# Optimization experiments

Measured on AMD Instinct MI355X. Metric: run time of the kernel, lower is better.

The kernel has to match this reference:

```python
import jax, jax.numpy as jnp
import numpy as np

DEVICE_DIM, SERVER_DIM, HIDDEN, HEAD_HIDDEN = 14, 3, 64, 128
B, N_DEV = 16384, 63
N_NODES = N_DEV + 1


def setup_inputs() -> dict:
    key = jax.random.key(0)
    ks = jax.random.split(key, 16)
    device_obs = jax.random.normal(ks[0], (B, N_DEV, DEVICE_DIM), dtype=jnp.float32)
    server_obs = jax.random.normal(ks[1], (B, SERVER_DIM), dtype=jnp.float32)
    # binary adjacency with self-loops (as built by _dense_adjacency_from_edge_index)
    rand = jax.random.uniform(ks[2], (B, N_NODES, N_NODES))
    adjacency = jnp.clip((rand < 0.3).astype(jnp.float32) + jnp.eye(N_NODES, dtype=jnp.float32), 0.0, 1.0)

    def lin(k, fan_in, fan_out):
        w = jax.random.normal(k, (fan_in, fan_out), dtype=jnp.float32) / np.sqrt(fan_in)
        return w

    return {
        'device_obs': device_obs,
        'server_obs': server_obs,
        'adjacency': adjacency,
        'W_dev': lin(ks[3], DEVICE_DIM, HIDDEN), 'b_dev': jnp.zeros((HIDDEN,), jnp.float32),
        'W_srv': lin(ks[4], SERVER_DIM, HIDDEN), 'b_srv': jnp.zeros((HIDDEN,), jnp.float32),
        'W1': lin(ks[5], HIDDEN, HIDDEN), 'b1': jnp.zeros((HIDDEN,), jnp.float32),
        'W2': lin(ks[6], HIDDEN, HIDDEN), 'b2': jnp.zeros((HIDDEN,), jnp.float32),
        'W3': lin(ks[7], HIDDEN, HIDDEN), 'b3': jnp.zeros((HIDDEN,), jnp.float32),
        'Wf1': lin(ks[8], HIDDEN * 3, HEAD_HIDDEN), 'bf1': jnp.zeros((HEAD_HIDDEN,), jnp.float32),
        'Wf2': lin(ks[9], HEAD_HIDDEN, 1), 'bf2': jnp.zeros((1,), jnp.float32),
    }


def _dense_gcn(x, adj_norm, W, b):
    # normalized adjacency matmul then linear: [B,N,N]@[B,N,H] -> [B,N,H]
    return jnp.einsum('bnm,bmh->bnh', adj_norm, x) @ W + b


def reference(device_obs, server_obs, adjacency,
              W_dev, b_dev, W_srv, b_srv,
              W1, b1, W2, b2, W3, b3,
              Wf1, bf1, Wf2, bf2):
    # node encoding
    device_emb = jax.nn.relu(device_obs @ W_dev + b_dev)            # [B,Nd,H]
    server_emb = jax.nn.relu(server_obs @ W_srv + b_srv)[:, None]   # [B,1,H]
    x = jnp.concatenate([device_emb, server_emb], axis=1)           # [B,N,H]

    # symmetric degree normalization D^-1/2 A D^-1/2 (degree clamped to >=1)
    degree = adjacency.sum(axis=-1)
    d_inv_sqrt = jnp.clip(degree, 1.0, None) ** -0.5
    adj_norm = d_inv_sqrt[:, :, None] * adjacency * d_inv_sqrt[:, None, :]

    h = jax.nn.relu(_dense_gcn(x, adj_norm, W1, b1))
    h = jax.nn.relu(_dense_gcn(h, adj_norm, W2, b2))
    h = jax.nn.relu(_dense_gcn(h, adj_norm, W3, b3))

    # head
    server_hidden = h[:, -1]                  # [B,H]
    device_hidden = h[:, :-1]                 # [B,Nd,H]
    dev_mean = device_hidden.mean(axis=1)     # [B,H]
    n = device_hidden.shape[1]
    shared_srv = jnp.broadcast_to(server_hidden[:, None], (h.shape[0], n, HIDDEN))
    shared_mean = jnp.broadcast_to(dev_mean[:, None], (h.shape[0], n, HIDDEN))
    critic_in = jnp.concatenate([device_hidden, shared_mean, shared_srv], axis=-1)  # [B,Nd,3H]
    out = jax.nn.relu(critic_in @ Wf1 + bf1) @ Wf2 + bf2
    return out[..., 0]  # [B,Nd]
```

## Files before the change

### kernel.cpp

```cpp
#include <hip/hip_runtime.h>
#include <hip/hip_bf16.h>
#include <stdint.h>

typedef __attribute__((ext_vector_type(8))) __bf16 bf16x8;
typedef __attribute__((ext_vector_type(4))) float f32x4;
typedef __attribute__((ext_vector_type(2))) float f32x2;
typedef __attribute__((ext_vector_type(4))) unsigned uint4v;
typedef __attribute__((ext_vector_type(2))) unsigned uint2v;

union U4 { uint4v u; bf16x8 b; };

#define WS_WDEV_H 0
#define WS_WDEV_L 4096
#define WS_W1_H   8192
#define WS_W1_L   16384
#define WS_W2_H   24576
#define WS_W2_L   32768
#define WS_W3_H   40960
#define WS_W3_L   49152
#define WS_WA_H   57344
#define WS_WA_L   73728
#define WS_WF_H   90112
#define WS_WF_L   122880

__device__ __forceinline__ unsigned short f2bf(float f){
  union { float f; unsigned u; } v; v.f = f;
  unsigned r = v.u + 0x7fffu + ((v.u >> 16) & 1u);
  return (unsigned short)(r >> 16);
}
__device__ __forceinline__ float bf2f(unsigned short h){
  union { unsigned u; float f; } v; v.u = ((unsigned)h) << 16; return v.f;
}
__device__ __forceinline__ void split2(float x, unsigned short& hi, unsigned short& lo){
  hi = f2bf(x);
  lo = f2bf(x - bf2f(hi));
}
__device__ __forceinline__ f32x4 mfma16(const U4& a, const U4& b, f32x4 c){
  return __builtin_amdgcn_mfma_f32_16x16x32_bf16(a.b, b.b, c, 0, 0, 0);
}

__device__ __forceinline__ unsigned cvt_pk_bf(float a, float b){
  float2 p; p.x = a; p.y = b;
  union { __hip_bfloat162 h; unsigned u; } cv;
  cv.h = __float22bfloat162_rn(p);
  return cv.u;
}
__device__ __forceinline__ void split_pair(float x0, float x1, unsigned& hi2, unsigned& lo2){
  hi2 = cvt_pk_bf(x0, x1);
  lo2 = cvt_pk_bf(x0 - __uint_as_float(hi2 << 16),
                  x1 - __uint_as_float(hi2 & 0xffff0000u));
}
__device__ __forceinline__ unsigned pack_hl(float z){
  unsigned h = cvt_pk_bf(z, 0.f) & 0xffffu;
  float r = z - __uint_as_float(h << 16);
  return (cvt_pk_bf(0.f, r) & 0xffff0000u) | h;
}

extern "C" __global__ void prep_weights(const float* __restrict__ Wdev,
                                        const float* __restrict__ W1,
                                        const float* __restrict__ W2,
                                        const float* __restrict__ W3,
                                        const float* __restrict__ Wf1,
                                        char* __restrict__ ws)
{
  unsigned short* WdevH = (unsigned short*)(ws + WS_WDEV_H);
  unsigned short* WdevL = (unsigned short*)(ws + WS_WDEV_L);
  unsigned short* WH[3] = {(unsigned short*)(ws+WS_W1_H),(unsigned short*)(ws+WS_W2_H),(unsigned short*)(ws+WS_W3_H)};
  unsigned short* WL[3] = {(unsigned short*)(ws+WS_W1_L),(unsigned short*)(ws+WS_W2_L),(unsigned short*)(ws+WS_W3_L)};
  unsigned short* WaH = (unsigned short*)(ws + WS_WA_H);
  unsigned short* WaL = (unsigned short*)(ws + WS_WA_L);
  unsigned short* WfH = (unsigned short*)(ws + WS_WF_H);
  unsigned short* WfL = (unsigned short*)(ws + WS_WF_L);
  const int total = 2048 + 3*4096 + 8192 + 16384;
  for (int idx = blockIdx.x*256 + threadIdx.x; idx < total; idx += gridDim.x*256){
    if (idx < 2048){
      int tt = idx;
      int frag = tt >> 9, within = tt & 511, lane = within >> 3, j = within & 7;
      int nt = frag & 3;
      int k = ((lane>>4)<<3) + j;
      int n = (nt<<4) + (lane & 15);
      float v = (k < 14) ? Wdev[k*64 + n] : 0.f;
      unsigned short h,l; split2(v,h,l); WdevH[tt]=h; WdevL[tt]=l;
    } else if (idx < 2048 + 3*4096){
      int tt = idx - 2048; int Li = tt / 4096; int r = tt - Li*4096;
      int frag = r >> 9, within = r & 511, lane = within >> 3, j = within & 7;
      int ks = frag >> 2, nt = frag & 3;
      int k = (ks<<5) + ((lane>>4)<<3) + j;
      int n = (nt<<4) + (lane & 15);
      const float* W = (Li==0) ? W1 : ((Li==1) ? W2 : W3);
      float v = W[k*64 + n];
      unsigned short h,l; split2(v,h,l); WH[Li][r]=h; WL[Li][r]=l;
    } else if (idx < 2048 + 3*4096 + 8192){
      int r = idx - (2048 + 3*4096);
      int frag = r >> 9, within = r & 511, lane = within >> 3, j = within & 7;
      int ks = frag >> 3, nt = frag & 7;
      int k = (ks<<5) + ((lane>>4)<<3) + j;
      int n = (nt<<4) + (lane & 15);
      float v = Wf1[k*128 + n];
      unsigned short h,l; split2(v,h,l); WaH[r]=h; WaL[r]=l;
    } else {
      int r = idx - (2048 + 3*4096 + 8192);
      int frag = r >> 9, within = r & 511, lane = within >> 3, j = within & 7;
      int ks = frag >> 3, nt = frag & 7;
      int k = (ks<<5) + ((lane>>4)<<3) + j;
      int n = (nt<<4) + (lane & 15);
      float v = Wf1[(64 + k)*128 + n];
      unsigned short h,l; split2(v,h,l); WfH[r]=h; WfL[r]=l;
    }
  }
}

extern "C" __global__ __launch_bounds__(256, 6)
void pgcn_fused(const float* __restrict__ dobs, const float* __restrict__ sobs,
                const float* __restrict__ adj,
                const float* __restrict__ bdev,
                const float* __restrict__ Wsrv, const float* __restrict__ bsrv,
                const float* __restrict__ b1, const float* __restrict__ b2,
                const float* __restrict__ b3,
                const float* __restrict__ bf1, const float* __restrict__ Wf2,
                const float* __restrict__ bf2,
                const char* __restrict__ ws, float* __restrict__ out)
{
  __shared__ __align__(16) unsigned short     lds_Yr[9216];
  __shared__ __align__(16) unsigned long long lds_Abits[64];
  __shared__ __align__(16) float    lds_d[64];
  __shared__ __align__(16) float    lds_mp[256];
  __shared__ __align__(16) float    lds_srv[64];
  __shared__ __align__(16) float    lds_s1[128];
  __shared__ __align__(16) unsigned short lds_Vh[128];
  __shared__ __align__(16) unsigned short lds_Vl[128];

  const int t = threadIdx.x;
  const int w = t >> 6;
  const int lane = t & 63;
  const int quad = lane >> 4;
  const int c = lane & 15;
  const long item = blockIdx.x;
  char* Yb = (char*)lds_Yr;

  {
    const f32x4* src = (const f32x4*)(adj + item*4096 + ((t>>2)<<6) + ((t&3)<<4));
    unsigned bits = 0;
    for (int i = 0; i < 4; ++i){
      f32x4 v = src[i];
      unsigned b = (v.x != 0.f) | (((unsigned)(v.y != 0.f))<<1)
                 | (((unsigned)(v.z != 0.f))<<2) | (((unsigned)(v.w != 0.f))<<3);
      bits |= b << (i<<2);
    }
    ((unsigned short*)lds_Abits)[t] = (unsigned short)bits;
  }

  unsigned ahi[4] = {0,0,0,0}, alo[4] = {0,0,0,0};
  {
    int m = (w<<4) + c;
    if (quad < 2 && m < 63){
      const float* rp = dobs + item*882 + m*14 + (quad<<3);
      float e[8];
      f32x2 p0 = *(const f32x2*)(rp);
      f32x2 p1 = *(const f32x2*)(rp+2);
      f32x2 p2 = *(const f32x2*)(rp+4);
      e[0]=p0.x; e[1]=p0.y; e[2]=p1.x; e[3]=p1.y; e[4]=p2.x; e[5]=p2.y;
      if (quad == 0){
        f32x2 p3 = *(const f32x2*)(rp+6);
        e[6]=p3.x; e[7]=p3.y;
      } else {
        e[6]=0.f; e[7]=0.f;
      }
      for (int d0 = 0; d0 < 4; ++d0)
        split_pair(e[2*d0], e[2*d0+1], ahi[d0], alo[d0]);
    }
  }
  __syncthreads();

  if (t < 64){
    unsigned long long mk = lds_Abits[t];
    int deg = __popcll(mk);
    lds_d[t] = 1.0f / sqrtf((float)(deg < 1 ? 1 : deg));
  }
  __syncthreads();

  f32x4 d4v = *(const f32x4*)&lds_d[(w<<4) + (quad<<2)];
  const float dd[4] = {d4v.x, d4v.y, d4v.z, d4v.w};
  const float ddc = lds_d[(w<<4) + c];

  U4 atk[2];
  {
    unsigned long long mk = lds_Abits[(w<<4) + c];
    for (int ks = 0; ks < 2; ++ks){
      unsigned byt = (unsigned)(mk >> ((ks<<5) + (quad<<3))) & 0xffu;
      for (int r = 0; r < 4; ++r){
        unsigned e = 0u - ((byt >> (2*r)) & 1u);
        unsigned o = 0u - ((byt >> (2*r+1)) & 1u);
        atk[ks].u[r] = (e & 0x3f80u) | (o & 0x3f800000u);
      }
    }
  }

  const int ybw = (c*72 + (w<<4) + (quad<<2)) << 1;
  const int yrd = (c*72 + (quad<<3)) << 1;
  const int zbw = (((w<<4)+c)*72 + (quad<<2)) << 1;
  const int zrd = (((w<<4)+c)*72 + (quad<<3)) << 1;

  float hcur[4][4];

  {
    U4 a_h, a_l;
    a_h.u = uint4v{ahi[0],ahi[1],ahi[2],ahi[3]};
    a_l.u = uint4v{alo[0],alo[1],alo[2],alo[3]};
    const uint4v* WdH = (const uint4v*)(ws + WS_WDEV_H);
    const uint4v* WdL = (const uint4v*)(ws + WS_WDEV_L);
    float srvv4[4];
    if (w == 3 && quad == 3){
      float s0 = sobs[item*3+0], s1v = sobs[item*3+1], s2v = sobs[item*3+2];
      for (int nt = 0; nt < 4; ++nt){
        int col = c + (nt<<4);
        float v = s0*Wsrv[col] + s1v*Wsrv[64+col] + s2v*Wsrv[128+col] + bsrv[col];
        srvv4[nt] = fmaxf(v, 0.f);
      }
    }
    for (int nt = 0; nt < 4; ++nt){
      U4 wh, wl;
      wh.u = WdH[(nt<<6) + lane];
      wl.u = WdL[(nt<<6) + lane];
      f32x4 g = {0.f,0.f,0.f,0.f};
      g = mfma16(a_h, wh, g);
      g = mfma16(a_h, wl, g);
      g = mfma16(a_l, wh, g);
      float bb = bdev[c + (nt<<4)];
      float y[4];
      for (int r = 0; r < 4; ++r) y[r] = fmaxf(g[r] + bb, 0.f);
      if (w == 3 && quad == 3) y[3] = srvv4[nt];
      for (int r = 0; r < 4; ++r) y[r] *= dd[r];
      unsigned h01, l01, h23, l23;
      split_pair(y[0], y[1], h01, l01);
      split_pair(y[2], y[3], h23, l23);
      *(uint2v*)(Yb + ybw + 2304*nt)        = uint2v{ h01, h23 };
      *(uint2v*)(Yb + ybw + 2304*nt + 9216) = uint2v{ l01, l23 };
    }
  }
  __syncthreads();

  const uint4v* WH_tab[3] = {(const uint4v*)(ws+WS_W1_H),(const uint4v*)(ws+WS_W2_H),(const uint4v*)(ws+WS_W3_H)};
  const uint4v* WL_tab[3] = {(const uint4v*)(ws+WS_W1_L),(const uint4v*)(ws+WS_W2_L),(const uint4v*)(ws+WS_W3_L)};
  const float* bias_tab[3] = {b1, b2, b3};

  for (int L = 0; L < 3; ++L){
    f32x4 zacc[4];
    for (int mt = 0; mt < 4; ++mt){
      f32x4 g = {0.f,0.f,0.f,0.f};
      for (int ks = 0; ks < 2; ++ks){
        U4 yh, yl;
        yh.u = *(const uint4v*)(Yb + yrd + 2304*mt + 64*ks);
        yl.u = *(const uint4v*)(Yb + yrd + 2304*mt + 64*ks + 9216);
        g = mfma16(yh, atk[ks], g);
        g = mfma16(yl, atk[ks], g);
      }
      zacc[mt] = g;
    }
    __syncthreads();

    for (int mt = 0; mt < 4; ++mt){
      unsigned h01, l01, h23, l23;
      split_pair(zacc[mt][0]*ddc, zacc[mt][1]*ddc, h01, l01);
      split_pair(zacc[mt][2]*ddc, zacc[mt][3]*ddc, h23, l23);
      *(uint2v*)(Yb + zbw + 32*mt)        = uint2v{ h01, h23 };
      *(uint2v*)(Yb + zbw + 32*mt + 9216) = uint2v{ l01, l23 };
    }
    __threadfence_block();
    U4 zh[2], zl[2];
    for (int ks = 0; ks < 2; ++ks){
      zh[ks].u = *(const uint4v*)(Yb + zrd + 64*ks);
      zl[ks].u = *(const uint4v*)(Yb + zrd + 64*ks + 9216);
    }

    const uint4v* WHp = WH_tab[L];
    const uint4v* WLp = WL_tab[L];
    const float* bp = bias_tab[L];
    for (int nt = 0; nt < 4; ++nt){
      f32x4 g = {0.f,0.f,0.f,0.f};
      for (int ks = 0; ks < 2; ++ks){
        U4 wh, wl;
        wh.u = WHp[((ks<<2)+nt)*64 + lane];
        wl.u = WLp[((ks<<2)+nt)*64 + lane];
        g = mfma16(zh[ks], wh, g);
        g = mfma16(zh[ks], wl, g);
        g = mfma16(zl[ks], wh, g);
      }
      float bb = bp[c + (nt<<4)];
      for (int r = 0; r < 4; ++r) hcur[nt][r] = fmaxf(g[r] + bb, 0.f);
    }
    __syncthreads();

    if (L < 2){
      for (int nt = 0; nt < 4; ++nt){
        unsigned h01, l01, h23, l23;
        split_pair(hcur[nt][0]*dd[0], hcur[nt][1]*dd[1], h01, l01);
        split_pair(hcur[nt][2]*dd[2], hcur[nt][3]*dd[3], h23, l23);
        *(uint2v*)(Yb + ybw + 2304*nt)        = uint2v{ h01, h23 };
        *(uint2v*)(Yb + ybw + 2304*nt + 9216) = uint2v{ l01, l23 };
      }
      __syncthreads();
    }
  }

  unsigned* zbuf = (unsigned*)Yb + (w<<10);
  const int piL = (lane>>2) | ((lane&3)<<4);
  const int s0L = (piL>>2) & 1;

  {
    bool isSrvLane = (w == 3) && (quad == 3);
    float cs[4];
    for (int nt = 0; nt < 4; ++nt){
      float s = hcur[nt][0] + hcur[nt][1] + hcur[nt][2] + hcur[nt][3];
      if (isSrvLane){ s -= hcur[nt][3]; lds_srv[c + (nt<<4)] = hcur[nt][3]; }
      s += __shfl_xor(s, 16);
      s += __shfl_xor(s, 32);
      cs[nt] = s;
    }
    if (quad == 0)
      for (int nt = 0; nt < 4; ++nt) lds_mp[(w<<6) + c + (nt<<4)] = cs[nt];
  }
  for (int nt = 0; nt < 4; ++nt){
    int ks = nt >> 1;
    int lcBase = (quad<<2) + ((((nt&1)<<1) + (c>>3)) << 4);
    int e = c & 7;
    for (int r = 0; r < 4; ++r){
      unsigned pk = pack_hl(hcur[nt][r]);
      int lane_c = lcBase + r;
      int pi = (lane_c>>2) | ((lane_c&3)<<4);
      int sel = ((e>>2) ^ (pi>>2)) & 1;
      zbuf[(ks<<9) + (pi<<3) + (sel<<2) + (e&3)] = pk;
    }
  }
  __syncthreads();

  if (t < 64){
    float mv = (lds_mp[t] + lds_mp[64+t] + lds_mp[128+t] + lds_mp[192+t]) * (1.0f/63.0f);
    unsigned short h,l; split2(mv,h,l);
    lds_Vh[t]=h; lds_Vl[t]=l;
  } else if (t < 128){
    float sv = lds_srv[t-64];
    unsigned short h,l; split2(sv,h,l);
    lds_Vh[t]=h; lds_Vl[t]=l;
  }
  __syncthreads();

  U4 hh[2], hl[2];
  for (int ks = 0; ks < 2; ++ks){
    uint4v qa = *(const uint4v*)&zbuf[(ks<<9) + (piL<<3) + (s0L<<2)];
    uint4v qb = *(const uint4v*)&zbuf[(ks<<9) + (piL<<3) + ((1-s0L)<<2)];
    hh[ks].u = uint4v{ (qa.y<<16)|(qa.x&0xffffu), (qa.w<<16)|(qa.z&0xffffu),
                       (qb.y<<16)|(qb.x&0xffffu), (qb.w<<16)|(qb.z&0xffffu) };
    hl[ks].u = uint4v{ (qa.y&0xffff0000u)|(qa.x>>16), (qa.w&0xffff0000u)|(qa.z>>16),
                       (qb.y&0xffff0000u)|(qb.x>>16), (qb.w&0xffff0000u)|(qb.z>>16) };
  }

  {
    const uint4v* WfH = (const uint4v*)(ws + WS_WF_H);
    const uint4v* WfL = (const uint4v*)(ws + WS_WF_L);
    f32x4 sacc0 = {0.f,0.f,0.f,0.f}, sacc1 = {0.f,0.f,0.f,0.f};
    for (int ks = 0; ks < 4; ++ks){
      U4 vh, vl;
      vh.u = *(const uint4v*)((const char*)lds_Vh + (ks<<6) + (quad<<4));
      vl.u = *(const uint4v*)((const char*)lds_Vl + (ks<<6) + (quad<<4));
      if (c != 0){ vh.u = uint4v{0,0,0,0}; vl.u = uint4v{0,0,0,0}; }
      int nt0 = (w<<1);
      U4 wh, wl;
      wh.u = WfH[((ks<<3)+nt0)*64 + lane];
      wl.u = WfL[((ks<<3)+nt0)*64 + lane];
      sacc0 = mfma16(vh, wh, sacc0);
      sacc0 = mfma16(vh, wl, sacc0);
      sacc0 = mfma16(vl, wh, sacc0);
      wh.u = WfH[((ks<<3)+nt0+1)*64 + lane];
      wl.u = WfL[((ks<<3)+nt0+1)*64 + lane];
      sacc1 = mfma16(vh, wh, sacc1);
      sacc1 = mfma16(vh, wl, sacc1);
      sacc1 = mfma16(vl, wh, sacc1);
    }
    if (quad == 0){
      int col0 = c + (w<<5);
      lds_s1[col0]      = sacc0[0] + bf1[col0];
      lds_s1[col0 + 16] = sacc1[0] + bf1[col0 + 16];
    }
  }
  __syncthreads();

  const uint4v* WaH = (const uint4v*)(ws + WS_WA_H);
  const uint4v* WaL = (const uint4v*)(ws + WS_WA_L);
  float outacc[4] = {0.f,0.f,0.f,0.f};
  for (int nt = 0; nt < 8; ++nt){
    f32x4 g = {0.f,0.f,0.f,0.f};
    for (int ks = 0; ks < 2; ++ks){
      U4 wh, wl;
      wh.u = WaH[((ks<<3)+nt)*64 + lane];
      wl.u = WaL[((ks<<3)+nt)*64 + lane];
      g = mfma16(hh[ks], wh, g);
      g = mfma16(hh[ks], wl, g);
      g = mfma16(hl[ks], wh, g);
    }
    int col = c + (nt<<4);
    float sv = lds_s1[col];
    float w2 = Wf2[col];
    for (int r = 0; r < 4; ++r){
      float zz = fmaxf(g[r] + sv, 0.f);
      outacc[r] += zz * w2;
    }
  }
  {
    float bb = bf2[0];
    for (int r = 0; r < 4; ++r){
      float v = outacc[r];
      v += __shfl_xor(v, 1); v += __shfl_xor(v, 2);
      v += __shfl_xor(v, 4); v += __shfl_xor(v, 8);
      if (c == 0){
        int row = (w<<4) + (quad<<2) + r;
        if (row < 63) out[item*63 + row] = v + bb;
      }
    }
  }
}

extern "C" void kernel_launch(void* const* d_in, const int* in_sizes, int n_in,
                              void* d_out, int out_size, void* d_ws, size_t ws_size,
                              hipStream_t stream)
{
  const float* dobs = (const float*)d_in[0];
  const float* sobs = (const float*)d_in[1];
  const float* adj  = (const float*)d_in[2];
  const float* Wdev = (const float*)d_in[3];
  const float* bdev = (const float*)d_in[4];
  const float* Wsrv = (const float*)d_in[5];
  const float* bsrv = (const float*)d_in[6];
  const float* W1   = (const float*)d_in[7];
  const float* b1   = (const float*)d_in[8];
  const float* W2   = (const float*)d_in[9];
  const float* b2   = (const float*)d_in[10];
  const float* W3   = (const float*)d_in[11];
  const float* b3   = (const float*)d_in[12];
  const float* Wf1  = (const float*)d_in[13];
  const float* bf1  = (const float*)d_in[14];
  const float* Wf2  = (const float*)d_in[15];
  const float* bf2  = (const float*)d_in[16];
  float* out = (float*)d_out;
  char* ws = (char*)d_ws;
  int nb = in_sizes[1] / 3;

  prep_weights<<<dim3(160), dim3(256), 0, stream>>>(Wdev, W1, W2, W3, Wf1, ws);
  pgcn_fused<<<dim3(nb), dim3(256), 0, stream>>>(dobs, sobs, adj, bdev, Wsrv, bsrv,
                                                 b1, b2, b3, bf1, Wf2, bf2, ws, out);
}
```

Baseline: 628.9 us.

## Software-pipeline weight and LDS loads with double buffering across GCN and head stages

Manually unrolls the embedding, GCN layer, and head MFMA loops so the weight fragments from the workspace and the LDS operands for the next tile load while the current tile's MFMAs run. Bias, Wf2, and server-encoding loads are hoisted earlier so their latency overlaps other work. The adjacency is read with nontemporal loads, and the block fence is replaced by an explicit lgkmcnt wait. The launch-bounds occupancy hint drops from 6 to 5 to leave room for the extra live registers, which may reduce latency hiding across waves.

```diff
diff --git a/kernel.cpp b/kernel.cpp
--- a/kernel.cpp
+++ b/kernel.cpp
@@ -110,7 +110,7 @@
   }
 }
 
-extern "C" __global__ __launch_bounds__(256, 6)
+extern "C" __global__ __launch_bounds__(256, 5)
 void pgcn_fused(const float* __restrict__ dobs, const float* __restrict__ sobs,
                 const float* __restrict__ adj,
                 const float* __restrict__ bdev,
@@ -137,12 +137,13 @@
   const int c = lane & 15;
   const long item = blockIdx.x;
   char* Yb = (char*)lds_Yr;
+  const bool isSrv = (w == 3) && (quad == 3);
 
   {
     const f32x4* src = (const f32x4*)(adj + item*4096 + ((t>>2)<<6) + ((t&3)<<4));
     unsigned bits = 0;
     for (int i = 0; i < 4; ++i){
-      f32x4 v = src[i];
+      f32x4 v = __builtin_nontemporal_load(src + i);
       unsigned b = (v.x != 0.f) | (((unsigned)(v.y != 0.f))<<1)
                  | (((unsigned)(v.z != 0.f))<<2) | (((unsigned)(v.w != 0.f))<<3);
       bits |= b << (i<<2);
@@ -170,6 +171,18 @@
         split_pair(e[2*d0], e[2*d0+1], ahi[d0], alo[d0]);
     }
   }
+
+  float bdv0 = bdev[c], bdv1 = bdev[c+16], bdv2 = bdev[c+32], bdv3 = bdev[c+48];
+  float srvv4[4];
+  if (isSrv){
+    float s0 = sobs[item*3+0], s1a = sobs[item*3+1], s2a = sobs[item*3+2];
+#pragma unroll
+    for (int nt = 0; nt < 4; ++nt){
+      int col = c + (nt<<4);
+      float v = s0*Wsrv[col] + s1a*Wsrv[64+col] + s2a*Wsrv[128+col] + bsrv[col];
+      srvv4[nt] = fmaxf(v, 0.f);
+    }
+  }
   __syncthreads();
 
   if (t < 64){
@@ -207,36 +220,34 @@
     U4 a_h, a_l;
     a_h.u = uint4v{ahi[0],ahi[1],ahi[2],ahi[3]};
     a_l.u = uint4v{alo[0],alo[1],alo[2],alo[3]};
-    const uint4v* WdH = (const uint4v*)(ws + WS_WDEV_H);
-    const uint4v* WdL = (const uint4v*)(ws + WS_WDEV_L);
-    float srvv4[4];
-    if (w == 3 && quad == 3){
-      float s0 = sobs[item*3+0], s1v = sobs[item*3+1], s2v = sobs[item*3+2];
-      for (int nt = 0; nt < 4; ++nt){
-        int col = c + (nt<<4);
-        float v = s0*Wsrv[col] + s1v*Wsrv[64+col] + s2v*Wsrv[128+col] + bsrv[col];
-        srvv4[nt] = fmaxf(v, 0.f);
-      }
-    }
-    for (int nt = 0; nt < 4; ++nt){
-      U4 wh, wl;
-      wh.u = WdH[(nt<<6) + lane];
-      wl.u = WdL[(nt<<6) + lane];
-      f32x4 g = {0.f,0.f,0.f,0.f};
-      g = mfma16(a_h, wh, g);
-      g = mfma16(a_h, wl, g);
-      g = mfma16(a_l, wh, g);
-      float bb = bdev[c + (nt<<4)];
-      float y[4];
-      for (int r = 0; r < 4; ++r) y[r] = fmaxf(g[r] + bb, 0.f);
-      if (w == 3 && quad == 3) y[3] = srvv4[nt];
-      for (int r = 0; r < 4; ++r) y[r] *= dd[r];
-      unsigned h01, l01, h23, l23;
-      split_pair(y[0], y[1], h01, l01);
-      split_pair(y[2], y[3], h23, l23);
-      *(uint2v*)(Yb + ybw + 2304*nt)        = uint2v{ h01, h23 };
-      *(uint2v*)(Yb + ybw + 2304*nt + 9216) = uint2v{ l01, l23 };
-    }
+    const uint4v* WdHp = (const uint4v*)(ws + WS_WDEV_H);
+    const uint4v* WdLp = (const uint4v*)(ws + WS_WDEV_L);
+    U4 eAh, eAl, eBh, eBl;
+    eAh.u = WdHp[0*64 + lane]; eAl.u = WdLp[0*64 + lane];
+    eBh.u = WdHp[1*64 + lane]; eBl.u = WdLp[1*64 + lane];
+#define EMB(NT, WHF, WLF, BB) { \
+    f32x4 g = {0.f,0.f,0.f,0.f}; \
+    g = mfma16(a_h, WHF, g); \
+    g = mfma16(a_h, WLF, g); \
+    g = mfma16(a_l, WHF, g); \
+    float y0 = fmaxf(g[0] + (BB), 0.f); \
+    float y1 = fmaxf(g[1] + (BB), 0.f); \
+    float y2 = fmaxf(g[2] + (BB), 0.f); \
+    float y3 = fmaxf(g[3] + (BB), 0.f); \
+    if (isSrv) y3 = srvv4[NT];             \
+    y0 *= dd[0]; y1 *= dd[1]; y2 *= dd[2]; y3 *= dd[3];    \
+    unsigned h01,l01,h23,l23; \
+    split_pair(y0, y1, h01, l01); \
+    split_pair(y2, y3, h23, l23); \
+    *(uint2v*)(Yb + ybw + 2304*(NT))        = uint2v{ h01, h23 }; \
+    *(uint2v*)(Yb + ybw + 2304*(NT) + 9216) = uint2v{ l01, l23 }; }
+    EMB(0, eAh, eAl, bdv0)
+    eAh.u = WdHp[2*64 + lane]; eAl.u = WdLp[2*64 + lane];
+    EMB(1, eBh, eBl, bdv1)
+    eBh.u = WdHp[3*64 + lane]; eBl.u = WdLp[3*64 + lane];
+    EMB(2, eAh, eAl, bdv2)
+    EMB(3, eBh, eBl, bdv3)
+#undef EMB
   }
   __syncthreads();
 
@@ -245,50 +256,90 @@
   const float* bias_tab[3] = {b1, b2, b3};
 
   for (int L = 0; L < 3; ++L){
-    f32x4 zacc[4];
-    for (int mt = 0; mt < 4; ++mt){
-      f32x4 g = {0.f,0.f,0.f,0.f};
-      for (int ks = 0; ks < 2; ++ks){
-        U4 yh, yl;
-        yh.u = *(const uint4v*)(Yb + yrd + 2304*mt + 64*ks);
-        yl.u = *(const uint4v*)(Yb + yrd + 2304*mt + 64*ks + 9216);
-        g = mfma16(yh, atk[ks], g);
-        g = mfma16(yl, atk[ks], g);
-      }
-      zacc[mt] = g;
-    }
-    __syncthreads();
-
-    for (int mt = 0; mt < 4; ++mt){
-      unsigned h01, l01, h23, l23;
-      split_pair(zacc[mt][0]*ddc, zacc[mt][1]*ddc, h01, l01);
-      split_pair(zacc[mt][2]*ddc, zacc[mt][3]*ddc, h23, l23);
-      *(uint2v*)(Yb + zbw + 32*mt)        = uint2v{ h01, h23 };
-      *(uint2v*)(Yb + zbw + 32*mt + 9216) = uint2v{ l01, l23 };
-    }
-    __threadfence_block();
-    U4 zh[2], zl[2];
-    for (int ks = 0; ks < 2; ++ks){
-      zh[ks].u = *(const uint4v*)(Yb + zrd + 64*ks);
-      zl[ks].u = *(const uint4v*)(Yb + zrd + 64*ks + 9216);
-    }
-
     const uint4v* WHp = WH_tab[L];
     const uint4v* WLp = WL_tab[L];
     const float* bp = bias_tab[L];
-    for (int nt = 0; nt < 4; ++nt){
-      f32x4 g = {0.f,0.f,0.f,0.f};
-      for (int ks = 0; ks < 2; ++ks){
-        U4 wh, wl;
-        wh.u = WHp[((ks<<2)+nt)*64 + lane];
-        wl.u = WLp[((ks<<2)+nt)*64 + lane];
-        g = mfma16(zh[ks], wh, g);
-        g = mfma16(zh[ks], wl, g);
-        g = mfma16(zl[ks], wh, g);
-      }
-      float bb = bp[c + (nt<<4)];
-      for (int r = 0; r < 4; ++r) hcur[nt][r] = fmaxf(g[r] + bb, 0.f);
-    }
+    float bL0 = bp[c], bL1 = bp[c+16], bL2 = bp[c+32], bL3 = bp[c+48];
+
+    f32x4 zacc0, zacc1, zacc2, zacc3;
+    {
+      U4 yAh0,yAl0,yAh1,yAl1, yBh0,yBl0,yBh1,yBl1;
+#define LOADY(H0,L0,H1,L1, MT) \
+      H0.u = *(const uint4v*)(Yb + yrd + 2304*(MT)); \
+      L0.u = *(const uint4v*)(Yb + yrd + 2304*(MT) + 9216); \
+      H1.u = *(const uint4v*)(Yb + yrd + 2304*(MT) + 64); \
+      L1.u = *(const uint4v*)(Yb + yrd + 2304*(MT) + 64 + 9216);
+#define ZSTEP(ZD, H0,L0,H1,L1) { \
+      f32x4 g = {0.f,0.f,0.f,0.f}; \
+      g = mfma16(H0, atk[0], g); \
+      g = mfma16(L0, atk[0], g); \
+      g = mfma16(H1, atk[1], g); \
+      g = mfma16(L1, atk[1], g); \
+      ZD = g; }
+      LOADY(yAh0,yAl0,yAh1,yAl1, 0)
+      LOADY(yBh0,yBl0,yBh1,yBl1, 1)
+      ZSTEP(zacc0, yAh0,yAl0,yAh1,yAl1)
+      LOADY(yAh0,yAl0,yAh1,yAl1, 2)
+      ZSTEP(zacc1, yBh0,yBl0,yBh1,yBl1)
+      LOADY(yBh0,yBl0,yBh1,yBl1, 3)
+      ZSTEP(zacc2, yAh0,yAl0,yAh1,yAl1)
+      ZSTEP(zacc3, yBh0,yBl0,yBh1,yBl1)
+#undef LOADY
+#undef ZSTEP
+    }
+    __syncthreads();
+
+    U4 wAh0,wAl0,wAh1,wAl1, wBh0,wBl0,wBh1,wBl1;
+#define LOADW(H0,L0,H1,L1, NT) \
+    H0.u = WHp[(NT)*64 + lane]; \
+    L0.u = WLp[(NT)*64 + lane]; \
+    H1.u = WHp[(4+(NT))*64 + lane]; \
+    L1.u = WLp[(4+(NT))*64 + lane];
+    LOADW(wAh0,wAl0,wAh1,wAl1, 0)
+
+    {
+      unsigned h01,l01,h23,l23;
+      split_pair(zacc0[0]*ddc, zacc0[1]*ddc, h01, l01);
+      split_pair(zacc0[2]*ddc, zacc0[3]*ddc, h23, l23);
+      *(uint2v*)(Yb + zbw +  0)        = uint2v{ h01, h23 };
+      *(uint2v*)(Yb + zbw +  0 + 9216) = uint2v{ l01, l23 };
+      split_pair(zacc1[0]*ddc, zacc1[1]*ddc, h01, l01);
+      split_pair(zacc1[2]*ddc, zacc1[3]*ddc, h23, l23);
+      *(uint2v*)(Yb + zbw + 32)        = uint2v{ h01, h23 };
+      *(uint2v*)(Yb + zbw + 32 + 9216) = uint2v{ l01, l23 };
+      split_pair(zacc2[0]*ddc, zacc2[1]*ddc, h01, l01);
+      split_pair(zacc2[2]*ddc, zacc2[3]*ddc, h23, l23);
+      *(uint2v*)(Yb + zbw + 64)        = uint2v{ h01, h23 };
+      *(uint2v*)(Yb + zbw + 64 + 9216) = uint2v{ l01, l23 };
+      split_pair(zacc3[0]*ddc, zacc3[1]*ddc, h01, l01);
+      split_pair(zacc3[2]*ddc, zacc3[3]*ddc, h23, l23);
+      *(uint2v*)(Yb + zbw + 96)        = uint2v{ h01, h23 };
+      *(uint2v*)(Yb + zbw + 96 + 9216) = uint2v{ l01, l23 };
+    }
+    asm volatile("s_waitcnt lgkmcnt(0)" ::: "memory");
+    U4 zh0, zl0, zh1, zl1;
+    zh0.u = *(const uint4v*)(Yb + zrd);
+    zl0.u = *(const uint4v*)(Yb + zrd + 9216);
+    zh1.u = *(const uint4v*)(Yb + zrd + 64);
+    zl1.u = *(const uint4v*)(Yb + zrd + 64 + 9216);
+
+    LOADW(wBh0,wBl0,wBh1,wBl1, 1)
+#define GSTEP(NT, H0,L0,H1,L1, BB) { \
+    f32x4 g = {0.f,0.f,0.f,0.f}; \
+    g = mfma16(zh0, H0, g); g = mfma16(zh0, L0, g); g = mfma16(zl0, H0, g); \
+    g = mfma16(zh1, H1, g); g = mfma16(zh1, L1, g); g = mfma16(zl1, H1, g); \
+    hcur[NT][0] = fmaxf(g[0] + (BB), 0.f); \
+    hcur[NT][1] = fmaxf(g[1] + (BB), 0.f); \
+    hcur[NT][2] = fmaxf(g[2] + (BB), 0.f); \
+    hcur[NT][3] = fmaxf(g[3] + (BB), 0.f); }
+    GSTEP(0, wAh0,wAl0,wAh1,wAl1, bL0)
+    LOADW(wAh0,wAl0,wAh1,wAl1, 2)
+    GSTEP(1, wBh0,wBl0,wBh1,wBl1, bL1)
+    LOADW(wBh0,wBl0,wBh1,wBl1, 3)
+    GSTEP(2, wAh0,wAl0,wAh1,wAl1, bL2)
+    GSTEP(3, wBh0,wBl0,wBh1,wBl1, bL3)
+#undef GSTEP
+#undef LOADW
     __syncthreads();
 
     if (L < 2){
@@ -308,11 +359,10 @@
   const int s0L = (piL>>2) & 1;
 
   {
-    bool isSrvLane = (w == 3) && (quad == 3);
     float cs[4];
     for (int nt = 0; nt < 4; ++nt){
       float s = hcur[nt][0] + hcur[nt][1] + hcur[nt][2] + hcur[nt][3];
-      if (isSrvLane){ s -= hcur[nt][3]; lds_srv[c + (nt<<4)] = hcur[nt][3]; }
+      if (isSrv){ s -= hcur[nt][3]; lds_srv[c + (nt<<4)] = hcur[nt][3]; }
       s += __shfl_xor(s, 16);
       s += __shfl_xor(s, 32);
       cs[nt] = s;
@@ -334,6 +384,11 @@
   }
   __syncthreads();
 
+  float wf2v[8];
+#pragma unroll
+  for (int nt = 0; nt < 8; ++nt) wf2v[nt] = Wf2[c + (nt<<4)];
+  const float bb2 = bf2[0];
+
   if (t < 64){
     float mv = (lds_mp[t] + lds_mp[64+t] + lds_mp[128+t] + lds_mp[192+t]) * (1.0f/63.0f);
     unsigned short h,l; split2(mv,h,l);
@@ -345,76 +400,110 @@
   }
   __syncthreads();
 
-  U4 hh[2], hl[2];
-  for (int ks = 0; ks < 2; ++ks){
-    uint4v qa = *(const uint4v*)&zbuf[(ks<<9) + (piL<<3) + (s0L<<2)];
-    uint4v qb = *(const uint4v*)&zbuf[(ks<<9) + (piL<<3) + ((1-s0L)<<2)];
-    hh[ks].u = uint4v{ (qa.y<<16)|(qa.x&0xffffu), (qa.w<<16)|(qa.z&0xffffu),
-                       (qb.y<<16)|(qb.x&0xffffu), (qb.w<<16)|(qb.z&0xffffu) };
-    hl[ks].u = uint4v{ (qa.y&0xffff0000u)|(qa.x>>16), (qa.w&0xffff0000u)|(qa.z>>16),
-                       (qb.y&0xffff0000u)|(qb.x>>16), (qb.w&0xffff0000u)|(qb.z>>16) };
-  }
-
-  {
-    const uint4v* WfH = (const uint4v*)(ws + WS_WF_H);
-    const uint4v* WfL = (const uint4v*)(ws + WS_WF_L);
+  U4 hh0, hh1, hl0, hl1;
+  {
+    uint4v qa0 = *(const uint4v*)&zbuf[(0<<9) + (piL<<3) + (s0L<<2)];
+    uint4v qb0 = *(const uint4v*)&zbuf[(0<<9) + (piL<<3) + ((1-s0L)<<2)];
+    uint4v qa1 = *(const uint4v*)&zbuf[(1<<9) + (piL<<3) + (s0L<<2)];
+    uint4v qb1 = *(const uint4v*)&zbuf[(1<<9) + (piL<<3) + ((1-s0L)<<2)];
+    hh0.u = uint4v{ (qa0.y<<16)|(qa0.x&0xffffu), (qa0.w<<16)|(qa0.z&0xffffu),
+                    (qb0.y<<16)|(qb0.x&0xffffu), (qb0.w<<16)|(qb0.z&0xffffu) };
+    hl0.u = uint4v{ (qa0.y&0xffff0000u)|(qa0.x>>16), (qa0.w&0xffff0000u)|(qa0.z>>16),
+                    (qb0.y&0xffff0000u)|(qb0.x>>16), (qb0.w&0xffff0000u)|(qb0.z>>16) };
+    hh1.u = uint4v{ (qa1.y<<16)|(qa1.x&0xffffu), (qa1.w<<16)|(qa1.z&0xffffu),
+                    (qb1.y<<16)|(qb1.x&0xffffu), (qb1.w<<16)|(qb1.z&0xffffu) };
+    hl1.u = uint4v{ (qa1.y&0xffff0000u)|(qa1.x>>16), (qa1.w&0xffff0000u)|(qa1.z>>16),
+                    (qb1.y&0xffff0000u)|(qb1.x>>16), (qb1.w&0xffff0000u)|(qb1.z>>16) };
+  }
+
+  {
+    const uint4v* WfHp = (const uint4v*)(ws + WS_WF_H);
+    const uint4v* WfLp = (const uint4v*)(ws + WS_WF_L);
+    const int nt0 = (w<<1);
+    float bf1a = 0.f, bf1b = 0.f;
+    if (quad == 0){ bf1a = bf1[c + (w<<5)]; bf1b = bf1[c + (w<<5) + 16]; }
     f32x4 sacc0 = {0.f,0.f,0.f,0.f}, sacc1 = {0.f,0.f,0.f,0.f};
-    for (int ks = 0; ks < 4; ++ks){
-      U4 vh, vl;
-      vh.u = *(const uint4v*)((const char*)lds_Vh + (ks<<6) + (quad<<4));
-      vl.u = *(const uint4v*)((const char*)lds_Vl + (ks<<6) + (quad<<4));
-      if (c != 0){ vh.u = uint4v{0,0,0,0}; vl.u = uint4v{0,0,0,0}; }
-      int nt0 = (w<<1);
-      U4 wh, wl;
-      wh.u = WfH[((ks<<3)+nt0)*64 + lane];
-      wl.u = WfL[((ks<<3)+nt0)*64 + lane];
-      sacc0 = mfma16(vh, wh, sacc0);
-      sacc0 = mfma16(vh, wl, sacc0);
-      sacc0 = mfma16(vl, wh, sacc0);
-      wh.u = WfH[((ks<<3)+nt0+1)*64 + lane];
-      wl.u = WfL[((ks<<3)+nt0+1)*64 + lane];
-      sacc1 = mfma16(vh, wh, sacc1);
-      sacc1 = mfma16(vh, wl, sacc1);
-      sacc1 = mfma16(vl, wh, sacc1);
-    }
+    U4 vAh,vAl, fA0,fA1,fA2,fA3;
+    U4 vBh,vBl, fB0,fB1,fB2,fB3;
+#define LOADS1(VH,VL,W0,W1,W2,W3, KS) \
+    VH.u = *(const uint4v*)((const char*)lds_Vh + ((KS)<<6) + (quad<<4)); \
+    VL.u = *(const uint4v*)((const char*)lds_Vl + ((KS)<<6) + (quad<<4)); \
+    if (c != 0){ VH.u = uint4v{0,0,0,0}; VL.u = uint4v{0,0,0,0}; } \
+    W0.u = WfHp[(((KS)<<3)+nt0)*64 + lane]; \
+    W1.u = WfLp[(((KS)<<3)+nt0)*64 + lane]; \
+    W2.u = WfHp[(((KS)<<3)+nt0+1)*64 + lane]; \
+    W3.u = WfLp[(((KS)<<3)+nt0+1)*64 + lane];
+#define S1STEP(VH,VL,W0,W1,W2,W3) \
+    sacc0 = mfma16(VH, W0, sacc0); sacc0 = mfma16(VH, W1, sacc0); sacc0 = mfma16(VL, W0, sacc0); \
+    sacc1 = mfma16(VH, W2, sacc1); sacc1 = mfma16(VH, W3, sacc1); sacc1 = mfma16(VL, W2, sacc1);
+    LOADS1(vAh,vAl,fA0,fA1,fA2,fA3, 0)
+    LOADS1(vBh,vBl,fB0,fB1,fB2,fB3, 1)
+    S1STEP(vAh,vAl,fA0,fA1,fA2,fA3)
+    LOADS1(vAh,vAl,fA0,fA1,fA2,fA3, 2)
+    S1STEP(vBh,vBl,fB0,fB1,fB2,fB3)
+    LOADS1(vBh,vBl,fB0,fB1,fB2,fB3, 3)
+    S1STEP(vAh,vAl,fA0,fA1,fA2,fA3)
+    S1STEP(vBh,vBl,fB0,fB1,fB2,fB3)
+#undef LOADS1
+#undef S1STEP
     if (quad == 0){
       int col0 = c + (w<<5);
-      lds_s1[col0]      = sacc0[0] + bf1[col0];
-      lds_s1[col0 + 16] = sacc1[0] + bf1[col0 + 16];
+      lds_s1[col0]      = sacc0[0] + bf1a;
+      lds_s1[col0 + 16] = sacc1[0] + bf1b;
     }
   }
   __syncthreads();
 
-  const uint4v* WaH = (const uint4v*)(ws + WS_WA_H);
-  const uint4v* WaL = (const uint4v*)(ws + WS_WA_L);
+  const uint4v* WaHp = (const uint4v*)(ws + WS_WA_H);
+  const uint4v* WaLp = (const uint4v*)(ws + WS_WA_L);
+  float s1v[8];
+#pragma unroll
+  for (int nt = 0; nt < 8; ++nt) s1v[nt] = lds_s1[c + (nt<<4)];
   float outacc[4] = {0.f,0.f,0.f,0.f};
-  for (int nt = 0; nt < 8; ++nt){
-    f32x4 g = {0.f,0.f,0.f,0.f};
-    for (int ks = 0; ks < 2; ++ks){
-      U4 wh, wl;
-      wh.u = WaH[((ks<<3)+nt)*64 + lane];
-      wl.u = WaL[((ks<<3)+nt)*64 + lane];
-      g = mfma16(hh[ks], wh, g);
-      g = mfma16(hh[ks], wl, g);
-      g = mfma16(hl[ks], wh, g);
-    }
-    int col = c + (nt<<4);
-    float sv = lds_s1[col];
-    float w2 = Wf2[col];
-    for (int r = 0; r < 4; ++r){
-      float zz = fmaxf(g[r] + sv, 0.f);
-      outacc[r] += zz * w2;
-    }
-  }
-  {
-    float bb = bf2[0];
+  {
+    U4 pAh0,pAl0,pAh1,pAl1, pBh0,pBl0,pBh1,pBl1;
+#define LOADWA(H0,L0,H1,L1, NT) \
+    H0.u = WaHp[(NT)*64 + lane]; \
+    L0.u = WaLp[(NT)*64 + lane]; \
+    H1.u = WaHp[(8+(NT))*64 + lane]; \
+    L1.u = WaLp[(8+(NT))*64 + lane];
+#define PSTEP(NT, H0,L0,H1,L1) { \
+    f32x4 g = {0.f,0.f,0.f,0.f}; \
+    g = mfma16(hh0, H0, g); g = mfma16(hh0, L0, g); g = mfma16(hl0, H0, g); \
+    g = mfma16(hh1, H1, g); g = mfma16(hh1, L1, g); g = mfma16(hl1, H1, g); \
+    float sv = s1v[NT]; float w2 = wf2v[NT]; \
+    outacc[0] += fmaxf(g[0] + sv, 0.f) * w2; \
+    outacc[1] += fmaxf(g[1] + sv, 0.f) * w2; \
+    outacc[2] += fmaxf(g[2] + sv, 0.f) * w2; \
+    outacc[3] += fmaxf(g[3] + sv, 0.f) * w2; }
+    LOADWA(pAh0,pAl0,pAh1,pAl1, 0)
+    LOADWA(pBh0,pBl0,pBh1,pBl1, 1)
+    PSTEP(0, pAh0,pAl0,pAh1,pAl1)
+    LOADWA(pAh0,pAl0,pAh1,pAl1, 2)
+    PSTEP(1, pBh0,pBl0,pBh1,pBl1)
+    LOADWA(pBh0,pBl0,pBh1,pBl1, 3)
+    PSTEP(2, pAh0,pAl0,pAh1,pAl1)
+    LOADWA(pAh0,pAl0,pAh1,pAl1, 4)
+    PSTEP(3, pBh0,pBl0,pBh1,pBl1)
+    LOADWA(pBh0,pBl0,pBh1,pBl1, 5)
+    PSTEP(4, pAh0,pAl0,pAh1,pAl1)
+    LOADWA(pAh0,pAl0,pAh1,pAl1, 6)
+    PSTEP(5, pBh0,pBl0,pBh1,pBl1)
+    LOADWA(pBh0,pBl0,pBh1,pBl1, 7)
+    PSTEP(6, pAh0,pAl0,pAh1,pAl1)
+    PSTEP(7, pBh0,pBl0,pBh1,pBl1)
+#undef PSTEP
+#undef LOADWA
+  }
+  {
+#pragma unroll
     for (int r = 0; r < 4; ++r){
       float v = outacc[r];
       v += __shfl_xor(v, 1); v += __shfl_xor(v, 2);
       v += __shfl_xor(v, 4); v += __shfl_xor(v, 8);
       if (c == 0){
         int row = (w<<4) + (quad<<2) + r;
-        if (row < 63) out[item*63 + row] = v + bb;
+        if (row < 63) out[item*63 + row] = v + bb2;
       }
     }
   }
```

Result: slower. 662.3 us (+5.3%).
